# Kernel optimization log

Hardware: AMD Instinct MI355X
Metric: run time of the kernel (lower is better)

Reference implementation:

```python
import jax, jax.numpy as jnp
import numpy as np

NUM_LAYERS = 4
INPUT_SIZE = 80
D_MODEL = 512
NHEAD = 8
D_FF = 2048
B = 16
S_MAX = 512
LN_EPS = 1e-5


def setup_inputs() -> dict:
    key = jax.random.key(0)
    ks = jax.random.split(key, 16)
    L, D, F, I = NUM_LAYERS, D_MODEL, D_FF, INPUT_SIZE
    s = 0.02
    inp = {
        "x": jax.random.normal(ks[0], (B, S_MAX, I), dtype=jnp.float32),
        "lens": jax.random.randint(ks[1], (B,), S_MAX // 2, S_MAX + 1, dtype=jnp.int32),
        "We": jax.random.normal(ks[2], (D, I), jnp.float32) * s,
        "be": jnp.zeros((D,), jnp.float32),
        "Wqkv": jax.random.normal(ks[3], (L, 3 * D, D), jnp.float32) * s,
        "bqkv": jnp.zeros((L, 3 * D), jnp.float32),
        "Wo": jax.random.normal(ks[4], (L, D, D), jnp.float32) * s,
        "bo": jnp.zeros((L, D), jnp.float32),
        "ln1_g": jnp.ones((L, D), jnp.float32),
        "ln1_b": jnp.zeros((L, D), jnp.float32),
        "W1": jax.random.normal(ks[5], (L, F, D), jnp.float32) * s,
        "b1": jnp.zeros((L, F), jnp.float32),
        "W2": jax.random.normal(ks[6], (L, D, F), jnp.float32) * s,
        "b2": jnp.zeros((L, D), jnp.float32),
        "ln2_g": jnp.ones((L, D), jnp.float32),
        "ln2_b": jnp.zeros((L, D), jnp.float32),
    }
    return inp


def _layer_norm(x, g, b):
    m = jnp.mean(x, axis=-1, keepdims=True)
    v = jnp.mean(jnp.square(x - m), axis=-1, keepdims=True)
    return (x - m) * jax.lax.rsqrt(v + LN_EPS) * g + b


def _pos_encoding(S, D, dtype):
    pos = jnp.arange(S, dtype=jnp.float32)[:, None]
    div = jnp.exp(jnp.arange(0, D, 2, dtype=jnp.float32) * (-np.log(10000.0) / D))
    pe = jnp.zeros((S, D), jnp.float32)
    pe = pe.at[:, 0::2].set(jnp.sin(pos * div))
    pe = pe.at[:, 1::2].set(jnp.cos(pos * div))
    return pe.astype(dtype)


def _encoder_layer(h, key_mask, Wqkv, bqkv, Wo, bo, g1, b1_, W1, b1f, W2, b2f, g2, b2_):
    # h: [B,S,D], key_mask: [B,S] bool (True = valid). Post-norm (PyTorch default).
    Bq, S, D = h.shape
    dh = D // NHEAD
    qkv = jnp.einsum("bsd,ed->bse", h, Wqkv) + bqkv  # [B,S,3D]
    q, k, v = jnp.split(qkv, 3, axis=-1)
    q = q.reshape(Bq, S, NHEAD, dh).transpose(0, 2, 1, 3)
    k = k.reshape(Bq, S, NHEAD, dh).transpose(0, 2, 1, 3)
    v = v.reshape(Bq, S, NHEAD, dh).transpose(0, 2, 1, 3)
    scores = jnp.einsum("bhqd,bhkd->bhqk", q, k) / jnp.sqrt(jnp.asarray(dh, h.dtype))
    scores = jnp.where(key_mask[:, None, None, :], scores, jnp.asarray(-1e9, h.dtype))
    attn = jax.nn.softmax(scores, axis=-1)
    ctx = jnp.einsum("bhqk,bhkd->bhqd", attn, v)
    ctx = ctx.transpose(0, 2, 1, 3).reshape(Bq, S, D)
    attn_out = jnp.einsum("bsd,ed->bse", ctx, Wo) + bo
    h = _layer_norm(h + attn_out, g1, b1_)
    ff = jnp.einsum("bsf,df->bsd", jax.nn.relu(jnp.einsum("bsd,fd->bsf", h, W1) + b1f), W2) + b2f
    return _layer_norm(h + ff, g2, b2_)


def reference(x, lens, We, be, Wqkv, bqkv, Wo, bo, ln1_g, ln1_b, W1, b1, W2, b2, ln2_g, ln2_b):
    Bq, S, _ = x.shape
    D = We.shape[0]
    h = jnp.einsum("bsi,di->bsd", x, We) + be  # Linear embedding
    h = h + _pos_encoding(S, D, h.dtype)[None]
    key_mask = jnp.arange(S)[None, :] < lens[:, None]  # [B,S]
    for l in range(Wqkv.shape[0]):
        h = _encoder_layer(h, key_mask, Wqkv[l], bqkv[l], Wo[l], bo[l],
                           ln1_g[l], ln1_b[l], W1[l], b1[l], W2[l], b2[l],
                           ln2_g[l], ln2_b[l])
    pooled = jnp.sum(h * key_mask[..., None].astype(h.dtype), axis=1)
    pooled = pooled / lens[:, None].astype(h.dtype)  # mean over valid tokens
    return pooled, lens
```

## Files before the change

kernel.cpp:

```cpp
#include <hip/hip_runtime.h>
#include <math.h>

#define D_MODEL 512
#define NHEAD   8
#define DH      64
#define D_FF    2048
#define BATCH   16
#define SMAX    512
#define NTOK    (BATCH*SMAX)
#define NLAYER  4

constexpr int MODE_QK   = 1;
constexpr int MODE_VT   = 2;
constexpr int MODE_RELU = 3;
constexpr int MODE_PART = 4;

typedef __attribute__((ext_vector_type(8))) __bf16 bf16x8;
typedef __attribute__((ext_vector_type(4))) float  f32x4;
typedef __attribute__((ext_vector_type(8))) int    i32x8;
typedef unsigned char u8;

#define WSCALE_INV 0.03125f

__device__ __forceinline__ unsigned short f2bf(float f) {
  union { float f; unsigned u; } v; v.f = f;
  unsigned r = v.u + 0x7FFFu + ((v.u >> 16) & 1u);
  return (unsigned short)(r >> 16);
}
__device__ __forceinline__ float bf2f(unsigned short u) {
  union { unsigned u; float f; } v; v.u = ((unsigned)u) << 16; return v.f;
}
__device__ __forceinline__ int pk4(float a, float b, float c, float d) {
  int t = __builtin_amdgcn_cvt_pk_fp8_f32(a, b, 0, false);
  t = __builtin_amdgcn_cvt_pk_fp8_f32(c, d, t, true);
  return t;
}

__device__ __forceinline__ void gl_lds16(const unsigned short* g, unsigned short* l) {
  __builtin_amdgcn_global_load_lds(
      (const __attribute__((address_space(1))) unsigned int*)g,
      (__attribute__((address_space(3)))       unsigned int*)l, 16, 0, 0);
}
__device__ __forceinline__ void gl_lds16b(const u8* g, u8* l) {
  __builtin_amdgcn_global_load_lds(
      (const __attribute__((address_space(1))) unsigned int*)g,
      (__attribute__((address_space(3)))       unsigned int*)l, 16, 0, 0);
}

__device__ __forceinline__ i32x8 ldfrag(const u8* base, int row, int q) {
  const int rx = row & 7;
  const int4 lo = *(const int4*)(base + (row << 7) + ((((2*q)    ) ^ rx) << 4));
  const int4 hi = *(const int4*)(base + (row << 7) + ((((2*q) + 1) ^ rx) << 4));
  union { int4 p[2]; i32x8 v; } u;
  u.p[0] = lo; u.p[1] = hi;
  return u.v;
}

template<int MODE>
__global__ __launch_bounds__(256)
void gemm_fp8(const u8* __restrict__ A, const u8* __restrict__ Bw,
              const float* __restrict__ bias, u8* __restrict__ C8,
              unsigned short* __restrict__ Cb,
              unsigned short* __restrict__ qd, unsigned short* __restrict__ kd,
              const int* __restrict__ lens, int K, int CK, int N)
{
  const int lin = blockIdx.x + gridDim.x*(blockIdx.y + gridDim.y*blockIdx.z);
  int m0, n0, kz = 0;
  if (MODE == MODE_VT) {
    n0 = (lin % gridDim.x) * 128;
    m0 = (lin / gridDim.x) * 128;
  } else {
    m0 = (lin % gridDim.y) * 128;
    const int rest = lin / gridDim.y;
    n0 = (rest % gridDim.x) * 128;
    kz = rest / gridDim.x;
  }
  if (MODE == MODE_VT) { if ((n0 & 511) >= lens[n0 >> 9]) return; }
  else                 { if ((m0 & 511) >= lens[m0 >> 9]) return; }

  __shared__ __attribute__((aligned(16))) u8 As[2][16384];
  __shared__ __attribute__((aligned(16))) u8 Bs[2][16384];
  const int tid  = threadIdx.x;
  const int lane = tid & 63;
  const int w    = tid >> 6;
  const int wm   = (w & 1) * 64;
  const int wn   = (w >> 1) * 64;
  const int l15  = lane & 15, quad = lane >> 4;

  f32x4 acc[4][4] = {};

  const int sr  = tid >> 3;
  const int sch = ((tid & 7) ^ (sr & 7)) * 16;
  const u8* Ag = A  + (long)(m0 + sr) * K + kz*CK + sch;
  const u8* Bg = Bw + (long)(n0 + sr) * K + kz*CK + sch;
  const long rowskip = (long)32 * K;
  const int t16 = tid * 16;
  const int niter = CK >> 7;

  auto stage = [&](int t, int bix) {
    const u8* a_ = Ag + t*128;
    const u8* b_ = Bg + t*128;
#pragma unroll
    for (int s = 0; s < 4; s++) {
      gl_lds16b(a_ + s*rowskip, &As[bix][s*4096 + t16]);
      gl_lds16b(b_ + s*rowskip, &Bs[bix][s*4096 + t16]);
    }
  };

  stage(0, 0);
  stage(1, 1);

  for (int it = 0; it < niter; ++it) {
    if (it + 1 < niter)
      asm volatile("s_waitcnt vmcnt(8)\n\ts_barrier" ::: "memory");
    else
      asm volatile("s_waitcnt vmcnt(0)\n\ts_barrier" ::: "memory");

    const int cur = it & 1;
    const u8* Ac = &As[cur][0];
    const u8* Bc = &Bs[cur][0];

    i32x8 bfv[4];
#pragma unroll
    for (int j = 0; j < 4; j++)
      bfv[j] = ldfrag(Bc, wn + j*16 + l15, quad);
#pragma unroll
    for (int i = 0; i < 4; i++) {
      const i32x8 af = ldfrag(Ac, wm + i*16 + l15, quad);
#pragma unroll
      for (int j = 0; j < 4; j++)
        acc[i][j] = __builtin_amdgcn_mfma_scale_f32_16x16x128_f8f6f4(
            af, bfv[j], acc[i][j], 0, 0, 0, 0x7F7F7F7F, 0, 0x7F7F7F7F);
    }

    if (it + 2 < niter) {
      __syncthreads();
      stage(it + 2, cur);
    }
  }

  __syncthreads();
  const int rr8 = lane >> 3, ch8 = lane & 7;

  if (MODE == MODE_RELU) {
    float* epf = (float*)&As[0][0] + w * 1088;
#pragma unroll
    for (int i = 0; i < 4; i++) {
#pragma unroll
      for (int j = 0; j < 4; j++) {
        const float cbv = bias[n0 + wn + j*16 + l15];
#pragma unroll
        for (int r = 0; r < 4; r++)
          epf[(quad*4 + r)*68 + j*16 + l15] = fmaxf(acc[i][j][r]*WSCALE_INV + cbv, 0.f);
      }
      asm volatile("s_waitcnt lgkmcnt(0)" ::: "memory");
      const int row = lane >> 2, c16 = (lane & 3) * 16;
      const float* rp = epf + row*68 + c16;
      f32x4 f0 = *(const f32x4*)(rp + 0);
      f32x4 f1 = *(const f32x4*)(rp + 4);
      f32x4 f2 = *(const f32x4*)(rp + 8);
      f32x4 f3 = *(const f32x4*)(rp + 12);
      int4 o;
      o.x = pk4(f0.x, f0.y, f0.z, f0.w);
      o.y = pk4(f1.x, f1.y, f1.z, f1.w);
      o.z = pk4(f2.x, f2.y, f2.z, f2.w);
      o.w = pk4(f3.x, f3.y, f3.z, f3.w);
      const int mrow = m0 + wm + i*16 + row;
      *(int4*)&C8[(long)mrow*N + n0 + wn + c16] = o;
      asm volatile("s_waitcnt lgkmcnt(0)" ::: "memory");
    }
  } else {
    unsigned short* epi = (unsigned short*)&As[0][0] + w * 1152;
    const bool isq = (MODE == MODE_QK) && (((n0 + wn) >> 9) == 0);
#pragma unroll
    for (int i = 0; i < 4; i++) {
      float rbv[4];
      if (MODE == MODE_VT) {
#pragma unroll
        for (int r = 0; r < 4; r++) rbv[r] = bias[m0 + wm + i*16 + quad*4 + r];
      }
#pragma unroll
      for (int j = 0; j < 4; j++) {
        float cbv = 0.f;
        if (MODE == MODE_QK) cbv = bias[n0 + wn + j*16 + l15];
#pragma unroll
        for (int r = 0; r < 4; r++) {
          float v = acc[i][j][r] * WSCALE_INV;
          if (MODE == MODE_QK)   { v += cbv; if (isq) v *= 0.125f; }
          if (MODE == MODE_VT)   v += rbv[r];
          epi[(quad*4 + r)*72 + j*16 + l15] = f2bf(v);
        }
      }
      asm volatile("s_waitcnt lgkmcnt(0)" ::: "memory");
#pragma unroll
      for (int rs = 0; rs < 2; rs++) {
        const int row  = rs*8 + rr8;
        const int mrow = m0 + wm + i*16 + row;
        bf16x8 val = *(const bf16x8*)&epi[row*72 + ch8*8];
        if (MODE == MODE_PART) {
          *(bf16x8*)&Cb[((long)kz*NTOK + mrow)*N + n0 + wn + ch8*8] = val;
        } else if (MODE == MODE_QK) {
          const int nb    = n0 + wn;
          const int which = nb >> 9;
          const int head  = (nb >> 6) & 7;
          unsigned short* dst = which ? kd : qd;
          const int bh = (mrow >> 9)*8 + head;
          *(bf16x8*)&dst[((long)(bh*512 + (mrow & 511)))*64 + ch8*8] = val;
        } else {
          const int head = mrow >> 6, d = mrow & 63;
          const int tok  = n0 + wn + ch8*8;
          const int b    = tok >> 9;
          *(bf16x8*)&Cb[((long)((b*8 + head)*64 + d))*512 + (tok & 511)] = val;
        }
      }
      asm volatile("s_waitcnt lgkmcnt(0)" ::: "memory");
    }
  }
}

template<int KS>
__global__ __launch_bounds__(128)
void reduce_ln(const unsigned short* __restrict__ part,
               const float* __restrict__ bias,
               const float* __restrict__ g, const float* __restrict__ bb,
               u8* __restrict__ h8, const int* __restrict__ lens)
{
  const int row = blockIdx.x, tid = threadIdx.x;
  if ((row & 511) >= lens[row >> 9]) return;
  const int hv = ((const int*)(h8 + (long)row*512))[tid];
  float4 bs = ((const float4*)bias)[tid];
  float v0 = __builtin_amdgcn_cvt_f32_fp8(hv, 0) + bs.x;
  float v1 = __builtin_amdgcn_cvt_f32_fp8(hv, 1) + bs.y;
  float v2 = __builtin_amdgcn_cvt_f32_fp8(hv, 2) + bs.z;
  float v3 = __builtin_amdgcn_cvt_f32_fp8(hv, 3) + bs.w;
#pragma unroll
  for (int z = 0; z < KS; z++) {
    ushort4 p = ((const ushort4*)(part + ((long)z*NTOK + row)*512))[tid];
    v0 += bf2f(p.x); v1 += bf2f(p.y); v2 += bf2f(p.z); v3 += bf2f(p.w);
  }
  float s  = v0 + v1 + v2 + v3;
  float s2 = v0*v0 + v1*v1 + v2*v2 + v3*v3;
#pragma unroll
  for (int off = 1; off < 64; off <<= 1) {
    s  += __shfl_xor(s, off);
    s2 += __shfl_xor(s2, off);
  }
  __shared__ float rb[4];
  if ((tid & 63) == 0) { rb[(tid>>6)*2] = s; rb[(tid>>6)*2+1] = s2; }
  __syncthreads();
  s = rb[0] + rb[2]; s2 = rb[1] + rb[3];
  const float mean = s * (1.f/512.f);
  const float var  = fmaxf(s2 * (1.f/512.f) - mean*mean, 0.f);
  const float rstd = rsqrtf(var + 1e-5f);
  const int e = tid*4;
  const float o0 = (v0-mean)*rstd*g[e+0] + bb[e+0];
  const float o1 = (v1-mean)*rstd*g[e+1] + bb[e+1];
  const float o2 = (v2-mean)*rstd*g[e+2] + bb[e+2];
  const float o3 = (v3-mean)*rstd*g[e+3] + bb[e+3];
  ((int*)(h8 + (long)row*512))[tid] = pk4(o0, o1, o2, o3);
}

__global__ __launch_bounds__(256)
void attn_mfma(const unsigned short* __restrict__ qg,
               const unsigned short* __restrict__ kb,
               const unsigned short* __restrict__ vtb,
               const int* __restrict__ lens,
               u8* __restrict__ ctx8)
{
  const int bh = blockIdx.x, qt = blockIdx.y;
  const int b = bh >> 3, hh = bh & 7;
  const int len = lens[b];
  if (qt*64 >= len) return;

  __shared__ __attribute__((aligned(16))) u8 smem[41984];
  unsigned short* Ks0 = (unsigned short*)smem;
  unsigned short* Vts0 = (unsigned short*)(smem + 16384);
  unsigned short* Ps  = (unsigned short*)(smem + 32768);
  const int tid = threadIdx.x;
  const int w = tid >> 6, lane = tid & 63, l15 = lane & 15, quad = lane >> 4;
  const int t8 = tid * 8;

  const int srow = tid >> 2;
  const int s8   = (tid & 3) * 8;
  const unsigned short* Kbase = kb  + ((long)(bh*512 + srow))*64 + s8;
  const unsigned short* Vbase = vtb + ((long)(bh*64 + srow))*512 + s8;

  const unsigned short* qrow = qg + ((long)(bh*512 + qt*64 + w*16 + l15))*64;
  const bf16x8 qf0 = *(const bf16x8*)(qrow + quad*8);
  const bf16x8 qf1 = *(const bf16x8*)(qrow + 32 + quad*8);

  f32x4 O[4] = {};
  float mrow[4] = {-1e30f,-1e30f,-1e30f,-1e30f};
  float lrow[4] = {0.f,0.f,0.f,0.f};
  unsigned short* Pw = &Ps[w*16*72];
  const int ntiles = (len + 63) >> 6;

  {
    gl_lds16(Kbase,      &Ks0[t8]);
    gl_lds16(Kbase + 32, &Ks0[2048 + t8]);
    gl_lds16(Vbase,      &Vts0[t8]);
    gl_lds16(Vbase + 32, &Vts0[2048 + t8]);
  }

  for (int kt = 0; kt < ntiles; kt++) {
    const int cur = kt & 1;
    unsigned short* Kc  = Ks0  + cur*4096;
    unsigned short* Vc  = Vts0 + cur*4096;
    __syncthreads();
    if (kt + 1 < ntiles) {
      const unsigned short* Kg = Kbase + (long)(kt+1)*64*64;
      const unsigned short* Vg = Vbase + (long)(kt+1)*64;
      unsigned short* Kn = Ks0  + (cur^1)*4096;
      unsigned short* Vn = Vts0 + (cur^1)*4096;
      gl_lds16(Kg,      &Kn[t8]);
      gl_lds16(Kg + 32, &Kn[2048 + t8]);
      gl_lds16(Vg,      &Vn[t8]);
      gl_lds16(Vg + 32, &Vn[2048 + t8]);
    }

    f32x4 sc[4];
#pragma unroll
    for (int ks = 0; ks < 4; ks++) {
      bf16x8 kf0 = *(const bf16x8*)&Kc[       (ks*16 + l15)*32 + quad*8];
      bf16x8 kf1 = *(const bf16x8*)&Kc[2048 + (ks*16 + l15)*32 + quad*8];
      f32x4 z = {};
      z = __builtin_amdgcn_mfma_f32_16x16x32_bf16(qf0, kf0, z, 0, 0, 0);
      sc[ks] = __builtin_amdgcn_mfma_f32_16x16x32_bf16(qf1, kf1, z, 0, 0, 0);
    }

    if (kt*64 + 64 > len) {
#pragma unroll
      for (int ks = 0; ks < 4; ks++) {
        const bool valid = (kt*64 + ks*16 + l15) < len;
#pragma unroll
        for (int r = 0; r < 4; r++)
          sc[ks][r] = valid ? sc[ks][r] : -1e30f;
      }
    }

    float pv[4][4];
#pragma unroll
    for (int r = 0; r < 4; r++) {
      float mx = fmaxf(fmaxf(sc[0][r], sc[1][r]), fmaxf(sc[2][r], sc[3][r]));
      mx = fmaxf(mx, __shfl_xor(mx, 1));
      mx = fmaxf(mx, __shfl_xor(mx, 2));
      mx = fmaxf(mx, __shfl_xor(mx, 4));
      mx = fmaxf(mx, __shfl_xor(mx, 8));
      const float newm  = fmaxf(mrow[r], mx);
      const float alpha = __expf(mrow[r] - newm);
      float ps = 0.f;
#pragma unroll
      for (int ks = 0; ks < 4; ks++) { pv[ks][r] = __expf(sc[ks][r] - newm); ps += pv[ks][r]; }
      ps += __shfl_xor(ps, 1); ps += __shfl_xor(ps, 2);
      ps += __shfl_xor(ps, 4); ps += __shfl_xor(ps, 8);
      lrow[r] = lrow[r]*alpha + ps;
      mrow[r] = newm;
#pragma unroll
      for (int d = 0; d < 4; d++) O[d][r] *= alpha;
    }

#pragma unroll
    for (int ks = 0; ks < 4; ks++)
#pragma unroll
      for (int r = 0; r < 4; r++)
        Pw[(quad*4 + r)*72 + ks*16 + l15] = f2bf(pv[ks][r]);
    asm volatile("s_waitcnt lgkmcnt(0)" ::: "memory");

    const bf16x8 pa0 = *(const bf16x8*)&Pw[l15*72 + quad*8];
    const bf16x8 pa1 = *(const bf16x8*)&Pw[l15*72 + 32 + quad*8];
#pragma unroll
    for (int d = 0; d < 4; d++) {
      bf16x8 vf0 = *(const bf16x8*)&Vc[       (d*16 + l15)*32 + quad*8];
      bf16x8 vf1 = *(const bf16x8*)&Vc[2048 + (d*16 + l15)*32 + quad*8];
      O[d] = __builtin_amdgcn_mfma_f32_16x16x32_bf16(pa0, vf0, O[d], 0, 0, 0);
      O[d] = __builtin_amdgcn_mfma_f32_16x16x32_bf16(pa1, vf1, O[d], 0, 0, 0);
    }
  }

  __syncthreads();
  float* epf = (float*)smem + w * 1088;
#pragma unroll
  for (int r = 0; r < 4; r++) {
    const float inv = 1.f / lrow[r];
#pragma unroll
    for (int d = 0; d < 4; d++)
      epf[(quad*4 + r)*68 + d*16 + l15] = O[d][r] * inv;
  }
  asm volatile("s_waitcnt lgkmcnt(0)" ::: "memory");
  {
    const int row = lane >> 2, c16 = (lane & 3) * 16;
    const float* rp = epf + row*68 + c16;
    f32x4 f0 = *(const f32x4*)(rp + 0);
    f32x4 f1 = *(const f32x4*)(rp + 4);
    f32x4 f2 = *(const f32x4*)(rp + 8);
    f32x4 f3 = *(const f32x4*)(rp + 12);
    int4 o;
    o.x = pk4(f0.x, f0.y, f0.z, f0.w);
    o.y = pk4(f1.x, f1.y, f1.z, f1.w);
    o.z = pk4(f2.x, f2.y, f2.z, f2.w);
    o.w = pk4(f3.x, f3.y, f3.z, f3.w);
    const long gaddr = (long)(b*512 + qt*64 + w*16 + row)*512 + hh*64 + c16;
    *(int4*)&ctx8[gaddr] = o;
  }
}

__global__ __launch_bounds__(256)
void pe_kernel(float* __restrict__ pe)
{
  const int i = blockIdx.x*256 + threadIdx.x;
  const int s = i >> 9, e = i & 511;
  const float dv  = __expf((float)(e & ~1) * (-9.210340371976184f / 512.0f));
  const float ang = (float)s * dv;
  pe[i] = (e & 1) ? cosf(ang) : sinf(ang);
}

__global__ __launch_bounds__(256)
void gemm_embed(const float* __restrict__ A, const float* __restrict__ Bm,
                const float* __restrict__ bias, const float* __restrict__ pe,
                u8* __restrict__ C8, int K, int N)
{
  __shared__ float As[8][132];
  __shared__ float Bs[8][68];
  const int tid = threadIdx.x;
  const int m0 = blockIdx.y * 128;
  const int n0 = blockIdx.x * 64;
  const int tx = tid & 15, ty = tid >> 4;
  const int a_k = tid & 7, a_m = tid >> 3;

  float acc[8][4] = {};
  const float* Ag = A  + (long)(m0 + a_m) * K + a_k;
  const float* Bg = Bm + (long)(n0 + a_m) * K + a_k;

  for (int k0 = 0; k0 < K; k0 += 8) {
#pragma unroll
    for (int i = 0; i < 4; i++)
      As[a_k][a_m + 32*i] = Ag[k0 + (long)32*i*K];
#pragma unroll
    for (int i = 0; i < 2; i++)
      Bs[a_k][a_m + 32*i] = Bg[k0 + (long)32*i*K];
    __syncthreads();
#pragma unroll
    for (int kk = 0; kk < 8; kk++) {
      float a[8], bv[4];
#pragma unroll
      for (int r = 0; r < 8; r++) a[r] = As[kk][ty*8 + r];
#pragma unroll
      for (int c = 0; c < 4; c++) bv[c] = Bs[kk][tx*4 + c];
#pragma unroll
      for (int r = 0; r < 8; r++)
#pragma unroll
        for (int c = 0; c < 4; c++)
          acc[r][c] += a[r] * bv[c];
    }
    __syncthreads();
  }

  const int n_base = n0 + tx*4;
#pragma unroll
  for (int r = 0; r < 8; r++) {
    int m = m0 + ty*8 + r;
    int s = m & 511;
    float4 pv = *(const float4*)(pe + (long)s*512 + n_base);
    int o = pk4(acc[r][0] + bias[n_base+0] + pv.x,
                acc[r][1] + bias[n_base+1] + pv.y,
                acc[r][2] + bias[n_base+2] + pv.z,
                acc[r][3] + bias[n_base+3] + pv.w);
    *(int*)(C8 + (long)m*N + n_base) = o;
  }
}

#define N4_QKV (NLAYER*3*D_MODEL*D_MODEL/4)
#define N4_WO  (NLAYER*D_MODEL*D_MODEL/4)
#define N4_W1  (NLAYER*D_FF*D_MODEL/4)
#define N4_W2  (NLAYER*D_MODEL*D_FF/4)
__global__ __launch_bounds__(256)
void cvt_all(const float* __restrict__ wq, const float* __restrict__ wo,
             const float* __restrict__ w1, const float* __restrict__ w2,
             u8* __restrict__ oq, u8* __restrict__ oo,
             u8* __restrict__ o1, u8* __restrict__ o2)
{
  int i = blockIdx.x*256 + threadIdx.x;
  const float* src; u8* dst; int off;
  if (i < N4_QKV)                          { src = wq; dst = oq; off = i; }
  else if (i < N4_QKV + N4_WO)             { src = wo; dst = oo; off = i - N4_QKV; }
  else if (i < N4_QKV + N4_WO + N4_W1)     { src = w1; dst = o1; off = i - N4_QKV - N4_WO; }
  else if (i < N4_QKV + N4_WO + N4_W1 + N4_W2) { src = w2; dst = o2; off = i - N4_QKV - N4_WO - N4_W1; }
  else return;
  float4 v = ((const float4*)src)[off];
  ((int*)dst)[off] = pk4(v.x*32.f, v.y*32.f, v.z*32.f, v.w*32.f);
}

__global__ __launch_bounds__(256)
void out_init(float* __restrict__ out, const int* __restrict__ lens)
{
  int i = blockIdx.x*256 + threadIdx.x;
  if (i < 8192) out[i] = 0.f;
  else if (i < 8192 + 16) out[i] = (float)lens[i - 8192];
}

__global__ __launch_bounds__(256)
void pool_kernel(const u8* __restrict__ h8,
                 const int* __restrict__ lens, float* __restrict__ out)
{
  const int b = blockIdx.y;
  const int s0 = blockIdx.x * 64;
  const int len = lens[b];
  if (s0 >= len) return;
  const int send = min(s0 + 64, len);
  const int tid = threadIdx.x;
  const int c = (tid & 127) * 4;
  const int half = tid >> 7;
  float a0 = 0.f, a1 = 0.f, a2 = 0.f, a3 = 0.f;
  for (int s = s0 + half; s < send; s += 2) {
    const int v = *(const int*)(h8 + ((long)(b*512 + s))*512 + c);
    a0 += __builtin_amdgcn_cvt_f32_fp8(v, 0);
    a1 += __builtin_amdgcn_cvt_f32_fp8(v, 1);
    a2 += __builtin_amdgcn_cvt_f32_fp8(v, 2);
    a3 += __builtin_amdgcn_cvt_f32_fp8(v, 3);
  }
  const float inv = 1.0f / (float)len;
  atomicAdd(out + b*512 + c + 0, a0 * inv);
  atomicAdd(out + b*512 + c + 1, a1 * inv);
  atomicAdd(out + b*512 + c + 2, a2 * inv);
  atomicAdd(out + b*512 + c + 3, a3 * inv);
}

extern "C" void kernel_launch(void* const* d_in, const int* in_sizes, int n_in,
                              void* d_out, int out_size, void* d_ws, size_t ws_size,
                              hipStream_t stream)
{
  const float* x    = (const float*)d_in[0];
  const int*   lens = (const int*)  d_in[1];
  const float* We   = (const float*)d_in[2];
  const float* be   = (const float*)d_in[3];
  const float* Wqkv = (const float*)d_in[4];
  const float* bqkv = (const float*)d_in[5];
  const float* Wo   = (const float*)d_in[6];
  const float* bo   = (const float*)d_in[7];
  const float* ln1g = (const float*)d_in[8];
  const float* ln1b = (const float*)d_in[9];
  const float* W1   = (const float*)d_in[10];
  const float* b1   = (const float*)d_in[11];
  const float* W2   = (const float*)d_in[12];
  const float* b2   = (const float*)d_in[13];
  const float* ln2g = (const float*)d_in[14];
  const float* ln2b = (const float*)d_in[15];
  float* out = (float*)d_out;

  const long TOK_D = (long)NTOK * D_MODEL;
  u8* base = (u8*)d_ws;
  float* pe = (float*)base;
  u8* h8    = base + 4*TOK_D;
  u8* ctx8  = h8   + TOK_D;
  u8* ff8   = ctx8 + TOK_D;
  unsigned short* q_b  = (unsigned short*)(ff8 + 4*TOK_D);
  unsigned short* k_b  = q_b + TOK_D;
  unsigned short* vt_b = k_b + TOK_D;
  unsigned short* part = vt_b + TOK_D;
  u8* wq8 = (u8*)(part + 4*TOK_D);
  u8* wo8 = wq8 + (long)NLAYER*3*D_MODEL*D_MODEL;
  u8* w18 = wo8 + (long)NLAYER*D_MODEL*D_MODEL;
  u8* w28 = w18 + (long)NLAYER*D_FF*D_MODEL;

  const dim3 blk(256);

  {
    const int n4tot = N4_QKV + N4_WO + N4_W1 + N4_W2;
    cvt_all<<<dim3((n4tot+255)/256), blk, 0, stream>>>(
        Wqkv, Wo, W1, W2, wq8, wo8, w18, w28);
    pe_kernel<<<dim3(512*512/256), blk, 0, stream>>>(pe);
  }

  gemm_embed<<<dim3(D_MODEL/64, NTOK/128), blk, 0, stream>>>(
      x, We, be, pe, h8, 80, D_MODEL);

  for (int l = 0; l < NLAYER; l++) {
    const u8* wq_l = wq8 + (long)l * 3*D_MODEL * D_MODEL;
    const u8* wo_l = wo8 + (long)l * D_MODEL * D_MODEL;
    const u8* w1_l = w18 + (long)l * D_FF * D_MODEL;
    const u8* w2_l = w28 + (long)l * D_MODEL * D_FF;
    const float* bqkv_l = bqkv + (long)l * 3*D_MODEL;
    const float* bo_l   = bo   + (long)l * D_MODEL;
    const float* b1_l   = b1   + (long)l * D_FF;
    const float* b2_l   = b2   + (long)l * D_MODEL;

    gemm_fp8<MODE_QK><<<dim3(2*D_MODEL/128, NTOK/128), blk, 0, stream>>>(
        h8, wq_l, bqkv_l, nullptr, nullptr, q_b, k_b, lens, D_MODEL, D_MODEL, 2*D_MODEL);

    gemm_fp8<MODE_VT><<<dim3(NTOK/128, D_MODEL/128), blk, 0, stream>>>(
        wq_l + (long)2*D_MODEL*D_MODEL, h8, bqkv_l + 2*D_MODEL, nullptr, vt_b,
        nullptr, nullptr, lens, D_MODEL, D_MODEL, NTOK);

    attn_mfma<<<dim3(NHEAD*BATCH, SMAX/64), blk, 0, stream>>>(
        q_b, k_b, vt_b, lens, ctx8);

    gemm_fp8<MODE_PART><<<dim3(D_MODEL/128, NTOK/128, 2), blk, 0, stream>>>(
        ctx8, wo_l, nullptr, nullptr, part, nullptr, nullptr, lens,
        D_MODEL, D_MODEL/2, D_MODEL);
    reduce_ln<2><<<dim3(NTOK), dim3(128), 0, stream>>>(
        part, bo_l, ln1g + l*D_MODEL, ln1b + l*D_MODEL, h8, lens);

    gemm_fp8<MODE_RELU><<<dim3(D_FF/128, NTOK/128), blk, 0, stream>>>(
        h8, w1_l, b1_l, ff8, nullptr, nullptr, nullptr, lens, D_MODEL, D_MODEL, D_FF);

    gemm_fp8<MODE_PART><<<dim3(D_MODEL/128, NTOK/128, 2), blk, 0, stream>>>(
        ff8, w2_l, nullptr, nullptr, part, nullptr, nullptr, lens,
        D_FF, D_FF/2, D_MODEL);
    reduce_ln<2><<<dim3(NTOK), dim3(128), 0, stream>>>(
        part, b2_l, ln2g + l*D_MODEL, ln2b + l*D_MODEL, h8, lens);
  }

  out_init<<<dim3((8192 + 16 + 255) / 256), blk, 0, stream>>>(out, lens);
  pool_kernel<<<dim3(SMAX/64, BATCH), blk, 0, stream>>>(h8, lens, out);
}
```

Before: 546.9 us.

## Fuse QKV GEMMs, drop online softmax max, compute positional encoding inline

Merges the Q/K and V-transpose projection GEMMs into one launch with a block-index split. Removes the running-max rescaling in attention by folding log2(e) into the Q scale and using exp2 with a fixed offset. Replaces the precomputed positional-encoding table with sincos computed in the embedding epilogue. The fixed softmax offset assumes bounded scores and could overflow or underflow for large activations.

```diff
diff --git a/kernel.cpp b/kernel.cpp
--- a/kernel.cpp
+++ b/kernel.cpp
@@ -21,6 +21,7 @@
 typedef unsigned char u8;
 
 #define WSCALE_INV 0.03125f
+#define QSCALE     0.18033688011112042f
 
 __device__ __forceinline__ unsigned short f2bf(float f) {
   union { float f; unsigned u; } v; v.f = f;
@@ -66,17 +67,13 @@
 {
   const int lin = blockIdx.x + gridDim.x*(blockIdx.y + gridDim.y*blockIdx.z);
   int m0, n0, kz = 0;
-  if (MODE == MODE_VT) {
-    n0 = (lin % gridDim.x) * 128;
-    m0 = (lin / gridDim.x) * 128;
-  } else {
+  {
     m0 = (lin % gridDim.y) * 128;
     const int rest = lin / gridDim.y;
     n0 = (rest % gridDim.x) * 128;
     kz = rest / gridDim.x;
   }
-  if (MODE == MODE_VT) { if ((n0 & 511) >= lens[n0 >> 9]) return; }
-  else                 { if ((m0 & 511) >= lens[m0 >> 9]) return; }
+  if ((m0 & 511) >= lens[m0 >> 9]) return;
 
   __shared__ __attribute__((aligned(16))) u8 As[2][16384];
   __shared__ __attribute__((aligned(16))) u8 Bs[2][16384];
@@ -171,23 +168,13 @@
     }
   } else {
     unsigned short* epi = (unsigned short*)&As[0][0] + w * 1152;
-    const bool isq = (MODE == MODE_QK) && (((n0 + wn) >> 9) == 0);
 #pragma unroll
     for (int i = 0; i < 4; i++) {
-      float rbv[4];
-      if (MODE == MODE_VT) {
-#pragma unroll
-        for (int r = 0; r < 4; r++) rbv[r] = bias[m0 + wm + i*16 + quad*4 + r];
-      }
 #pragma unroll
       for (int j = 0; j < 4; j++) {
-        float cbv = 0.f;
-        if (MODE == MODE_QK) cbv = bias[n0 + wn + j*16 + l15];
 #pragma unroll
         for (int r = 0; r < 4; r++) {
           float v = acc[i][j][r] * WSCALE_INV;
-          if (MODE == MODE_QK)   { v += cbv; if (isq) v *= 0.125f; }
-          if (MODE == MODE_VT)   v += rbv[r];
           epi[(quad*4 + r)*72 + j*16 + l15] = f2bf(v);
         }
       }
@@ -197,24 +184,136 @@
         const int row  = rs*8 + rr8;
         const int mrow = m0 + wm + i*16 + row;
         bf16x8 val = *(const bf16x8*)&epi[row*72 + ch8*8];
-        if (MODE == MODE_PART) {
-          *(bf16x8*)&Cb[((long)kz*NTOK + mrow)*N + n0 + wn + ch8*8] = val;
-        } else if (MODE == MODE_QK) {
-          const int nb    = n0 + wn;
-          const int which = nb >> 9;
-          const int head  = (nb >> 6) & 7;
-          unsigned short* dst = which ? kd : qd;
-          const int bh = (mrow >> 9)*8 + head;
-          *(bf16x8*)&dst[((long)(bh*512 + (mrow & 511)))*64 + ch8*8] = val;
-        } else {
-          const int head = mrow >> 6, d = mrow & 63;
-          const int tok  = n0 + wn + ch8*8;
-          const int b    = tok >> 9;
-          *(bf16x8*)&Cb[((long)((b*8 + head)*64 + d))*512 + (tok & 511)] = val;
-        }
+        *(bf16x8*)&Cb[((long)kz*NTOK + mrow)*N + n0 + wn + ch8*8] = val;
       }
       asm volatile("s_waitcnt lgkmcnt(0)" ::: "memory");
     }
+  }
+}
+
+__global__ __launch_bounds__(256)
+void gemm_qkv(const u8* __restrict__ h8, const u8* __restrict__ wq,
+              const float* __restrict__ bqkv,
+              unsigned short* __restrict__ qd, unsigned short* __restrict__ kd,
+              unsigned short* __restrict__ vt_b,
+              const int* __restrict__ lens)
+{
+  const int lin = blockIdx.x;
+  const bool isVT = lin >= 512;
+  int m0, n0;
+  if (isVT) { const int idx = lin - 512; n0 = (idx & 63) * 128; m0 = (idx >> 6) * 128; }
+  else      { m0 = (lin & 63) * 128;     n0 = (lin >> 6) * 128; }
+  { const int tb = isVT ? n0 : m0;
+    if ((tb & 511) >= lens[tb >> 9]) return; }
+
+  const u8* Ap = isVT ? (wq + (long)2*D_MODEL*D_MODEL) : h8;
+  const u8* Bp = isVT ? h8 : wq;
+
+  __shared__ __attribute__((aligned(16))) u8 As[2][16384];
+  __shared__ __attribute__((aligned(16))) u8 Bs[2][16384];
+  const int tid  = threadIdx.x;
+  const int lane = tid & 63;
+  const int w    = tid >> 6;
+  const int wm   = (w & 1) * 64;
+  const int wn   = (w >> 1) * 64;
+  const int l15  = lane & 15, quad = lane >> 4;
+
+  f32x4 acc[4][4] = {};
+
+  const int sr  = tid >> 3;
+  const int sch = ((tid & 7) ^ (sr & 7)) * 16;
+  const u8* Ag = Ap + (long)(m0 + sr) * 512 + sch;
+  const u8* Bg = Bp + (long)(n0 + sr) * 512 + sch;
+  const long rowskip = (long)32 * 512;
+  const int t16 = tid * 16;
+
+  auto stage = [&](int t, int bix) {
+    const u8* a_ = Ag + t*128;
+    const u8* b_ = Bg + t*128;
+#pragma unroll
+    for (int s = 0; s < 4; s++) {
+      gl_lds16b(a_ + s*rowskip, &As[bix][s*4096 + t16]);
+      gl_lds16b(b_ + s*rowskip, &Bs[bix][s*4096 + t16]);
+    }
+  };
+
+  stage(0, 0);
+  stage(1, 1);
+
+#pragma unroll 1
+  for (int it = 0; it < 4; ++it) {
+    if (it + 1 < 4)
+      asm volatile("s_waitcnt vmcnt(8)\n\ts_barrier" ::: "memory");
+    else
+      asm volatile("s_waitcnt vmcnt(0)\n\ts_barrier" ::: "memory");
+
+    const int cur = it & 1;
+    const u8* Ac = &As[cur][0];
+    const u8* Bc = &Bs[cur][0];
+
+    i32x8 bfv[4];
+#pragma unroll
+    for (int j = 0; j < 4; j++)
+      bfv[j] = ldfrag(Bc, wn + j*16 + l15, quad);
+#pragma unroll
+    for (int i = 0; i < 4; i++) {
+      const i32x8 af = ldfrag(Ac, wm + i*16 + l15, quad);
+#pragma unroll
+      for (int j = 0; j < 4; j++)
+        acc[i][j] = __builtin_amdgcn_mfma_scale_f32_16x16x128_f8f6f4(
+            af, bfv[j], acc[i][j], 0, 0, 0, 0x7F7F7F7F, 0, 0x7F7F7F7F);
+    }
+
+    if (it + 2 < 4) {
+      __syncthreads();
+      stage(it + 2, cur);
+    }
+  }
+
+  __syncthreads();
+  const int rr8 = lane >> 3, ch8 = lane & 7;
+  unsigned short* epi = (unsigned short*)&As[0][0] + w * 1152;
+  const bool isq = !isVT && (((n0 + wn) >> 9) == 0);
+#pragma unroll
+  for (int i = 0; i < 4; i++) {
+    float rbv[4];
+    if (isVT) {
+#pragma unroll
+      for (int r = 0; r < 4; r++) rbv[r] = bqkv[2*D_MODEL + m0 + wm + i*16 + quad*4 + r];
+    }
+#pragma unroll
+    for (int j = 0; j < 4; j++) {
+      float cbv = 0.f;
+      if (!isVT) cbv = bqkv[n0 + wn + j*16 + l15];
+#pragma unroll
+      for (int r = 0; r < 4; r++) {
+        float v = acc[i][j][r] * WSCALE_INV;
+        if (!isVT) { v += cbv; if (isq) v *= QSCALE; }
+        else       v += rbv[r];
+        epi[(quad*4 + r)*72 + j*16 + l15] = f2bf(v);
+      }
+    }
+    asm volatile("s_waitcnt lgkmcnt(0)" ::: "memory");
+#pragma unroll
+    for (int rs = 0; rs < 2; rs++) {
+      const int row  = rs*8 + rr8;
+      const int mrow = m0 + wm + i*16 + row;
+      bf16x8 val = *(const bf16x8*)&epi[row*72 + ch8*8];
+      if (!isVT) {
+        const int nb    = n0 + wn;
+        const int which = nb >> 9;
+        const int head  = (nb >> 6) & 7;
+        unsigned short* dst = which ? kd : qd;
+        const int bh = (mrow >> 9)*8 + head;
+        *(bf16x8*)&dst[((long)(bh*512 + (mrow & 511)))*64 + ch8*8] = val;
+      } else {
+        const int head = mrow >> 6, d = mrow & 63;
+        const int tok  = n0 + wn + ch8*8;
+        const int b    = tok >> 9;
+        *(bf16x8*)&vt_b[((long)((b*8 + head)*64 + d))*512 + (tok & 511)] = val;
+      }
+    }
+    asm volatile("s_waitcnt lgkmcnt(0)" ::: "memory");
   }
 }
 
@@ -290,7 +389,6 @@
   const bf16x8 qf1 = *(const bf16x8*)(qrow + 32 + quad*8);
 
   f32x4 O[4] = {};
-  float mrow[4] = {-1e30f,-1e30f,-1e30f,-1e30f};
   float lrow[4] = {0.f,0.f,0.f,0.f};
   unsigned short* Pw = &Ps[w*16*72];
   const int ntiles = (len + 63) >> 6;
@@ -340,24 +438,13 @@
 
     float pv[4][4];
 #pragma unroll
-    for (int r = 0; r < 4; r++) {
-      float mx = fmaxf(fmaxf(sc[0][r], sc[1][r]), fmaxf(sc[2][r], sc[3][r]));
-      mx = fmaxf(mx, __shfl_xor(mx, 1));
-      mx = fmaxf(mx, __shfl_xor(mx, 2));
-      mx = fmaxf(mx, __shfl_xor(mx, 4));
-      mx = fmaxf(mx, __shfl_xor(mx, 8));
-      const float newm  = fmaxf(mrow[r], mx);
-      const float alpha = __expf(mrow[r] - newm);
-      float ps = 0.f;
-#pragma unroll
-      for (int ks = 0; ks < 4; ks++) { pv[ks][r] = __expf(sc[ks][r] - newm); ps += pv[ks][r]; }
-      ps += __shfl_xor(ps, 1); ps += __shfl_xor(ps, 2);
-      ps += __shfl_xor(ps, 4); ps += __shfl_xor(ps, 8);
-      lrow[r] = lrow[r]*alpha + ps;
-      mrow[r] = newm;
-#pragma unroll
-      for (int d = 0; d < 4; d++) O[d][r] *= alpha;
-    }
+    for (int ks = 0; ks < 4; ks++)
+#pragma unroll
+      for (int r = 0; r < 4; r++) {
+        const float p = exp2f(sc[ks][r] - 16.f);
+        pv[ks][r] = p;
+        lrow[r] += p;
+      }
 
 #pragma unroll
     for (int ks = 0; ks < 4; ks++)
@@ -375,6 +462,16 @@
       O[d] = __builtin_amdgcn_mfma_f32_16x16x32_bf16(pa0, vf0, O[d], 0, 0, 0);
       O[d] = __builtin_amdgcn_mfma_f32_16x16x32_bf16(pa1, vf1, O[d], 0, 0, 0);
     }
+  }
+
+#pragma unroll
+  for (int r = 0; r < 4; r++) {
+    float t = lrow[r];
+    t += __shfl_xor(t, 1);
+    t += __shfl_xor(t, 2);
+    t += __shfl_xor(t, 4);
+    t += __shfl_xor(t, 8);
+    lrow[r] = t;
   }
 
   __syncthreads();
@@ -405,18 +502,8 @@
 }
 
 __global__ __launch_bounds__(256)
-void pe_kernel(float* __restrict__ pe)
-{
-  const int i = blockIdx.x*256 + threadIdx.x;
-  const int s = i >> 9, e = i & 511;
-  const float dv  = __expf((float)(e & ~1) * (-9.210340371976184f / 512.0f));
-  const float ang = (float)s * dv;
-  pe[i] = (e & 1) ? cosf(ang) : sinf(ang);
-}
-
-__global__ __launch_bounds__(256)
 void gemm_embed(const float* __restrict__ A, const float* __restrict__ Bm,
-                const float* __restrict__ bias, const float* __restrict__ pe,
+                const float* __restrict__ bias,
                 u8* __restrict__ C8, int K, int N)
 {
   __shared__ float As[8][132];
@@ -456,15 +543,21 @@
   }
 
   const int n_base = n0 + tx*4;
+  const float cfreq = -13.287712379549449f / 512.0f;
+  const float dv0 = exp2f((float)(n_base)     * cfreq);
+  const float dv1 = exp2f((float)(n_base + 2) * cfreq);
 #pragma unroll
   for (int r = 0; r < 8; r++) {
     int m = m0 + ty*8 + r;
     int s = m & 511;
-    float4 pv = *(const float4*)(pe + (long)s*512 + n_base);
-    int o = pk4(acc[r][0] + bias[n_base+0] + pv.x,
-                acc[r][1] + bias[n_base+1] + pv.y,
-                acc[r][2] + bias[n_base+2] + pv.z,
-                acc[r][3] + bias[n_base+3] + pv.w);
+    float a0 = (float)s * dv0, a1 = (float)s * dv1;
+    float s0v, c0v, s1v, c1v;
+    __sincosf(a0, &s0v, &c0v);
+    __sincosf(a1, &s1v, &c1v);
+    int o = pk4(acc[r][0] + bias[n_base+0] + s0v,
+                acc[r][1] + bias[n_base+1] + c0v,
+                acc[r][2] + bias[n_base+2] + s1v,
+                acc[r][3] + bias[n_base+3] + c1v);
     *(int*)(C8 + (long)m*N + n_base) = o;
   }
 }
@@ -549,7 +642,6 @@
 
   const long TOK_D = (long)NTOK * D_MODEL;
   u8* base = (u8*)d_ws;
-  float* pe = (float*)base;
   u8* h8    = base + 4*TOK_D;
   u8* ctx8  = h8   + TOK_D;
   u8* ff8   = ctx8 + TOK_D;
@@ -568,11 +660,10 @@
     const int n4tot = N4_QKV + N4_WO + N4_W1 + N4_W2;
     cvt_all<<<dim3((n4tot+255)/256), blk, 0, stream>>>(
         Wqkv, Wo, W1, W2, wq8, wo8, w18, w28);
-    pe_kernel<<<dim3(512*512/256), blk, 0, stream>>>(pe);
   }
 
   gemm_embed<<<dim3(D_MODEL/64, NTOK/128), blk, 0, stream>>>(
-      x, We, be, pe, h8, 80, D_MODEL);
+      x, We, be, h8, 80, D_MODEL);
 
   for (int l = 0; l < NLAYER; l++) {
     const u8* wq_l = wq8 + (long)l * 3*D_MODEL * D_MODEL;
@@ -584,12 +675,8 @@
     const float* b1_l   = b1   + (long)l * D_FF;
     const float* b2_l   = b2   + (long)l * D_MODEL;
 
-    gemm_fp8<MODE_QK><<<dim3(2*D_MODEL/128, NTOK/128), blk, 0, stream>>>(
-        h8, wq_l, bqkv_l, nullptr, nullptr, q_b, k_b, lens, D_MODEL, D_MODEL, 2*D_MODEL);
-
-    gemm_fp8<MODE_VT><<<dim3(NTOK/128, D_MODEL/128), blk, 0, stream>>>(
-        wq_l + (long)2*D_MODEL*D_MODEL, h8, bqkv_l + 2*D_MODEL, nullptr, vt_b,
-        nullptr, nullptr, lens, D_MODEL, D_MODEL, NTOK);
+    gemm_qkv<<<dim3(768), blk, 0, stream>>>(
+        h8, wq_l, bqkv_l, q_b, k_b, vt_b, lens);
 
     attn_mfma<<<dim3(NHEAD*BATCH, SMAX/64), blk, 0, stream>>>(
         q_b, k_b, vt_b, lens, ctx8);
```

Result: faster. 495.3 us (-9.4%).
